# Optimization experiments

Measured on AMD Instinct MI355X. Metric: run time of the kernel, lower is better.

The kernel has to match this reference:

```python
import jax, jax.numpy as jnp
import numpy as np
from jax import lax

NUM_GROUP = 512
GROUP_SIZE = 32


def setup_inputs() -> dict:
    key = jax.random.key(0)
    xyz = jax.random.normal(key, (8, 8192, 6), dtype=jnp.float32)
    return {"xyz": xyz}


def _fps_indices(pts, K):
    """Farthest point sampling. pts: [B,N,3] -> idx [B,K] int32. Start at point 0."""
    B, N, _ = pts.shape
    first = jnp.zeros((B,), dtype=jnp.int32)
    # squared distance of every point to the first selected point
    d = jnp.sum((pts - pts[:, :1, :]) ** 2, axis=-1)  # [B,N]

    def step(d, _):
        nxt = jnp.argmax(d, axis=1).astype(jnp.int32)              # [B]
        newp = jnp.take_along_axis(pts, nxt[:, None, None], axis=1)  # [B,1,3]
        d = jnp.minimum(d, jnp.sum((pts - newp) ** 2, axis=-1))
        return d, nxt

    _, rest = lax.scan(step, d, None, length=K - 1)  # rest: [K-1,B]
    idx = jnp.concatenate([first[None, :], rest], axis=0)  # [K,B]
    return idx.T  # [B,K]


def _group(xyz, num_group, group_size):
    coords = xyz[:, :, :3]    # [B,N,3]
    normals = xyz[:, :, 3:6]  # [B,N,3]

    fps_idx = _fps_indices(coords, num_group)                          # [B,G]
    center = jnp.take_along_axis(coords, fps_idx[:, :, None], axis=1)  # [B,G,3]

    # pairwise squared distances center->points: [B,G,N]
    c2 = jnp.sum(center ** 2, axis=-1)[:, :, None]
    x2 = jnp.sum(coords ** 2, axis=-1)[:, None, :]
    cx = jnp.einsum('bgd,bnd->bgn', center, coords)
    d2 = c2 - 2.0 * cx + x2

    _, knn_idx = lax.top_k(-d2, group_size)  # [B,G,M] nearest neighbors

    flat_idx = knn_idx.reshape(knn_idx.shape[0], -1)  # [B,G*M]
    neigh = jnp.take_along_axis(coords, flat_idx[:, :, None], axis=1)
    neigh = neigh.reshape(-1, num_group, group_size, 3) - center[:, :, None, :]
    neigh_n = jnp.take_along_axis(normals, flat_idx[:, :, None], axis=1)
    neigh_n = neigh_n.reshape(-1, num_group, group_size, 3)
    return neigh, neigh_n, center


def reference(xyz):
    return _group(xyz, NUM_GROUP, GROUP_SIZE)
```

## Files before the change

### kernel.cpp

```cpp
#include <hip/hip_runtime.h>
#include <stdint.h>

#define BATCH 8
#define NPTS 8192
#define NGRP 512
#define GSZ 32
#define NWORK 248
#define CHUNK 16
typedef unsigned long long u64;
typedef float vf2 __attribute__((ext_vector_type(2)));

__device__ __forceinline__ float sq3(float dx, float dy, float dz) {
    return __fadd_rn(__fadd_rn(__fmul_rn(dx, dx), __fmul_rn(dy, dy)), __fmul_rn(dz, dz));
}

template <int C>
__device__ __forceinline__ float dpp_max_f32_step(float v) {
    const int t = __builtin_amdgcn_update_dpp(__float_as_int(v), __float_as_int(v),
                                              C, 0xF, 0xF, false);
    return fmaxf(v, __int_as_float(t));
}
template <int C>
__device__ __forceinline__ unsigned dpp_min_u32_step(unsigned v) {
    const unsigned t = (unsigned)__builtin_amdgcn_update_dpp((int)v, (int)v,
                                                             C, 0xF, 0xF, false);
    return v < t ? v : t;
}
__device__ __forceinline__ float wave_max_f32(float v) {
    v = dpp_max_f32_step<0x111>(v);
    v = dpp_max_f32_step<0x112>(v);
    v = dpp_max_f32_step<0x114>(v);
    v = dpp_max_f32_step<0x118>(v);
    v = dpp_max_f32_step<0x142>(v);
    v = dpp_max_f32_step<0x143>(v);
    return __int_as_float(__builtin_amdgcn_readlane(__float_as_int(v), 63));
}
__device__ __forceinline__ unsigned wave_min_u32(unsigned v) {
    v = dpp_min_u32_step<0x111>(v);
    v = dpp_min_u32_step<0x112>(v);
    v = dpp_min_u32_step<0x114>(v);
    v = dpp_min_u32_step<0x118>(v);
    v = dpp_min_u32_step<0x142>(v);
    v = dpp_min_u32_step<0x143>(v);
    return (unsigned)__builtin_amdgcn_readlane((int)v, 63);
}

__global__ void zero_rc(unsigned* __restrict__ rc) {
    if (threadIdx.x < BATCH) rc[threadIdx.x] = 0;
}

__global__ __launch_bounds__(512) void fused_kernel(const float* __restrict__ xyz,
                                                    float* __restrict__ centers,
                                                    float* __restrict__ neigh,
                                                    float* __restrict__ neigh_n,
                                                    unsigned* __restrict__ rc,
                                                    unsigned* __restrict__ cpx,
                                                    unsigned* __restrict__ cpy,
                                                    unsigned* __restrict__ cpz) {
    __shared__ float4 P4[NPTS];
    __shared__ double pkey[2][8];
    __shared__ float cl[NGRP * 3];
    __shared__ u64 rk[2][8];
    __shared__ int sel[GSZ];

    const int wid = blockIdx.x;
    const int tid = threadIdx.x;
    const int lane = tid & 63;
    const int wv = tid >> 6;

    if (wid < BATCH) {
        const int b = wid;
        vf2 px[8], py[8], pz[8], d2[8];
        const float* base = xyz + (size_t)b * NPTS * 6;

#pragma unroll
        for (int i = 0; i < 16; ++i) {
            const int p = i * 512 + tid;
            const float4 v4 = *reinterpret_cast<const float4*>(base + (size_t)p * 6);
            px[i >> 1][i & 1] = v4.x; py[i >> 1][i & 1] = v4.y; pz[i >> 1][i & 1] = v4.z;
            d2[i >> 1][i & 1] = __int_as_float(0x7f800000);
            P4[p] = make_float4(v4.x, v4.y, v4.z, 0.0f);
        }
        float Bx = base[0], By = base[1], Bz = base[2];
        if (tid == 0) { cl[0] = Bx; cl[1] = By; cl[2] = Bz; }
        __syncthreads();

        for (int k = 1; k < NGRP; ++k) {
            {
#pragma clang fp contract(off)
                const vf2 bx2 = {Bx, Bx}, by2 = {By, By}, bz2 = {Bz, Bz};
#pragma unroll
                for (int j = 0; j < 8; ++j) {
                    const vf2 dx = px[j] - bx2;
                    const vf2 dy = py[j] - by2;
                    const vf2 dz = pz[j] - bz2;
                    const vf2 mx2 = dx * dx;
                    const vf2 my2 = dy * dy;
                    const vf2 mz2 = dz * dz;
                    const vf2 s = (mx2 + my2) + mz2;
                    d2[j] = __builtin_elementwise_min(d2[j], s);
                }
            }
            vf2 mv = d2[0];
#pragma unroll
            for (int j = 1; j < 8; ++j) mv = __builtin_elementwise_max(mv, d2[j]);
            const float mx = fmaxf(mv[0], mv[1]);
            const float wmx = wave_max_f32(mx);
            int wi = 0;
#pragma unroll
            for (int i = 15; i >= 1; --i) {
                wi = (d2[i >> 1][i & 1] == mx) ? i : wi;
            }
            unsigned widx_w;
            const u64 bal = __ballot(mx == wmx);
            if (__popcll(bal) == 1) {
                const int L = __ffsll(bal) - 1;
                widx_w = (unsigned)(__builtin_amdgcn_readlane(wi, L) * 512 + (wv * 64 + L));
            } else {
                const unsigned cand = (mx == wmx) ? (unsigned)(wi * 512 + tid) : 0xFFFFFFFFu;
                widx_w = wave_min_u32(cand);
            }

            const int buf = k & 1;
            if ((tid & 63) == 0) {
                pkey[buf][wv] = __hiloint2double(__float_as_int(wmx), 8191 - (int)widx_w);
            }
            __syncthreads();

            const double2* pp = reinterpret_cast<const double2*>(&pkey[buf][0]);
            const double2 a = pp[0], c = pp[1], e = pp[2], f = pp[3];
            const double g = fmax(fmax(fmax(a.x, a.y), fmax(c.x, c.y)),
                                  fmax(fmax(e.x, e.y), fmax(f.x, f.y)));
            const int widx = 8191 - __double2loint(g);
            const float4 c4 = P4[widx];
            Bx = c4.x; By = c4.y; Bz = c4.z;

            if (tid == 0) {
                cl[k * 3 + 0] = Bx; cl[k * 3 + 1] = By; cl[k * 3 + 2] = Bz;
                if ((k & (CHUNK - 1)) == (CHUNK - 1)) {
                    const int k0 = k - (CHUNK - 1);
#pragma unroll
                    for (int j = 0; j < CHUNK; ++j) {
                        const int kk = k0 + j;
                        const int gi = b * NGRP + kk;
                        __hip_atomic_store(&cpx[gi], __float_as_uint(cl[kk * 3 + 0]),
                                           __ATOMIC_RELAXED, __HIP_MEMORY_SCOPE_AGENT);
                        __hip_atomic_store(&cpy[gi], __float_as_uint(cl[kk * 3 + 1]),
                                           __ATOMIC_RELAXED, __HIP_MEMORY_SCOPE_AGENT);
                        __hip_atomic_store(&cpz[gi], __float_as_uint(cl[kk * 3 + 2]),
                                           __ATOMIC_RELAXED, __HIP_MEMORY_SCOPE_AGENT);
                    }
                    __hip_atomic_store(&rc[b], (unsigned)(k + 1),
                                       __ATOMIC_RELEASE, __HIP_MEMORY_SCOPE_AGENT);
                }
            }
        }

        __syncthreads();
        float* cg = centers + (size_t)b * NGRP * 3;
        for (int t = tid; t < NGRP * 3; t += 512) cg[t] = cl[t];

    } else {
        for (int t = wid - BATCH; t < BATCH * NGRP; t += NWORK) {
            const int b = t & 7, g = t >> 3;
            if (tid == 0) {
                while (__hip_atomic_load(&rc[b], __ATOMIC_ACQUIRE,
                                         __HIP_MEMORY_SCOPE_AGENT) <= (unsigned)g) {
                    __builtin_amdgcn_s_sleep(2);
                }
            }
            __syncthreads();

            const int gi = b * NGRP + g;
            const float cx = __uint_as_float(__hip_atomic_load(
                &cpx[gi], __ATOMIC_RELAXED, __HIP_MEMORY_SCOPE_AGENT));
            const float cy = __uint_as_float(__hip_atomic_load(
                &cpy[gi], __ATOMIC_RELAXED, __HIP_MEMORY_SCOPE_AGENT));
            const float cz = __uint_as_float(__hip_atomic_load(
                &cpz[gi], __ATOMIC_RELAXED, __HIP_MEMORY_SCOPE_AGENT));
            const float c2 = sq3(cx, cy, cz);

            const float* base = xyz + (size_t)b * NPTS * 6;
            u64 key[16];
#pragma unroll
            for (int i = 0; i < 16; ++i) {
                const int p = i * 512 + tid;
                const float4 v4 = *reinterpret_cast<const float4*>(base + (size_t)p * 6);
                const float x = v4.x, y = v4.y, z = v4.z;
                const float x2 = sq3(x, y, z);
                const float dot = __fmaf_rn(cz, z, __fmaf_rn(cy, y, __fmul_rn(cx, x)));
                const float dd = __fadd_rn(__fsub_rn(c2, __fmul_rn(2.0f, dot)), x2);
                unsigned u = __float_as_uint(dd);
                u ^= (unsigned)(((int)u >> 31)) | 0x80000000u;
                key[i] = ((u64)u << 32) | (unsigned)p;
            }

            u64 lm = ~0ULL, lm2v = ~0ULL;
#pragma unroll
            for (int i = 0; i < 16; ++i) {
                const u64 kk = key[i];
                const bool a = kk < lm;
                const bool b2 = kk < lm2v;
                lm2v = a ? lm : (b2 ? kk : lm2v);
                lm = a ? kk : lm;
            }

            for (int r = 0; r < GSZ; ++r) {
                const unsigned hi = (unsigned)(lm >> 32);
                const unsigned minhi = wave_min_u32(hi);
                unsigned minlo;
                const u64 bal = __ballot(hi == minhi);
                if (__popcll(bal) == 1) {
                    const int L = __ffsll(bal) - 1;
                    minlo = (unsigned)__builtin_amdgcn_readlane((int)(unsigned)lm, L);
                } else {
                    const unsigned cand = (hi == minhi) ? (unsigned)lm : 0xFFFFFFFFu;
                    minlo = wave_min_u32(cand);
                }
                const u64 mk = ((u64)minhi << 32) | minlo;

                const int rb = r & 1;
                if (lane == 0) rk[rb][wv] = mk;
                __syncthreads();
                const ulonglong2* rp = reinterpret_cast<const ulonglong2*>(&rk[rb][0]);
                const ulonglong2 r0 = rp[0], r1 = rp[1], r2 = rp[2], r3 = rp[3];
                const u64 m0 = r0.x < r0.y ? r0.x : r0.y;
                const u64 m1 = r1.x < r1.y ? r1.x : r1.y;
                const u64 m2 = r2.x < r2.y ? r2.x : r2.y;
                const u64 m3 = r3.x < r3.y ? r3.x : r3.y;
                const u64 m01 = m0 < m1 ? m0 : m1;
                const u64 m23 = m2 < m3 ? m2 : m3;
                const u64 gm = m01 < m23 ? m01 : m23;
                if (tid == 0) sel[r] = (int)(unsigned)(gm & 0xffffffffu);
                if (lm == gm) {
                    if (lm2v != 0ULL) {
                        lm = lm2v;
                    } else {
                        u64 nm = ~0ULL;
#pragma unroll
                        for (int i = 0; i < 16; ++i) {
                            const u64 v = key[i] > gm ? key[i] : ~0ULL;
                            nm = v < nm ? v : nm;
                        }
                        lm = nm;
                    }
                    lm2v = 0ULL;
                }
            }
            __syncthreads();

            if (tid < GSZ) {
                const int idx = sel[tid];
                const float* q = base + (size_t)idx * 6;
                const float4 a4 = *reinterpret_cast<const float4*>(q);
                const float2 b2v = *reinterpret_cast<const float2*>(q + 4);
                const int row = b * NGRP + g;
                const size_t o = ((size_t)row * GSZ + tid) * 3;
                neigh[o + 0] = __fsub_rn(a4.x, cx);
                neigh[o + 1] = __fsub_rn(a4.y, cy);
                neigh[o + 2] = __fsub_rn(a4.z, cz);
                neigh_n[o + 0] = a4.w;
                neigh_n[o + 1] = b2v.x;
                neigh_n[o + 2] = b2v.y;
            }
        }
    }
}

extern "C" void kernel_launch(void* const* d_in, const int* in_sizes, int n_in,
                              void* d_out, int out_size, void* d_ws, size_t ws_size,
                              hipStream_t stream) {
    const float* xyz = (const float*)d_in[0];
    float* out = (float*)d_out;
    float* neigh   = out;
    float* neigh_n = out + (size_t)BATCH * NGRP * GSZ * 3;
    float* centers = out + (size_t)2 * BATCH * NGRP * GSZ * 3;

    unsigned* rc  = (unsigned*)d_ws;
    unsigned* cpx = (unsigned*)((char*)d_ws + 1024);
    unsigned* cpy = (unsigned*)((char*)d_ws + 1024 + 16384);
    unsigned* cpz = (unsigned*)((char*)d_ws + 1024 + 32768);

    zero_rc<<<1, 64, 0, stream>>>(rc);
    fused_kernel<<<BATCH + NWORK, 512, 0, stream>>>(xyz, centers, neigh, neigh_n,
                                                    rc, cpx, cpy, cpz);
}
```

Before: 547.9 us.

## Publish FPS centers in parallel with lagged release and fewer consumer blocks

The FPS producer now publishes each finished chunk of centers from 48 threads in parallel, using an interleaved xyz buffer instead of three separate arrays. It releases the ready counter one chunk late, taking the serial per-center stores off thread 0's critical path inside the FPS loop. Consumer blocks drop from 248 to 120 and back off longer while polling, which cuts memory traffic from spinning that could slow the latency-bound FPS loop. The trade-off is fewer workers for the kNN phase and later availability of each center chunk, which could lengthen the tail after FPS finishes.

```diff
diff --git a/kernel.cpp b/kernel.cpp
--- a/kernel.cpp
+++ b/kernel.cpp
@@ -5,7 +5,7 @@
 #define NPTS 8192
 #define NGRP 512
 #define GSZ 32
-#define NWORK 248
+#define NWORK 120
 #define CHUNK 16
 typedef unsigned long long u64;
 typedef float vf2 __attribute__((ext_vector_type(2)));
@@ -54,9 +54,7 @@
                                                     float* __restrict__ neigh,
                                                     float* __restrict__ neigh_n,
                                                     unsigned* __restrict__ rc,
-                                                    unsigned* __restrict__ cpx,
-                                                    unsigned* __restrict__ cpy,
-                                                    unsigned* __restrict__ cpz) {
+                                                    unsigned* __restrict__ cp) {
     __shared__ float4 P4[NPTS];
     __shared__ double pkey[2][8];
     __shared__ float cl[NGRP * 3];
@@ -127,6 +125,18 @@
             }
             __syncthreads();
 
+            if ((k & (CHUNK - 1)) == 0) {
+                if (tid == 0 && k >= 2 * CHUNK) {
+                    __hip_atomic_store(&rc[b], (unsigned)(k - CHUNK),
+                                       __ATOMIC_RELEASE, __HIP_MEMORY_SCOPE_AGENT);
+                }
+                if (tid < 3 * CHUNK) {
+                    const int j = (k - CHUNK) * 3 + tid;
+                    __hip_atomic_store(&cp[b * NGRP * 3 + j], __float_as_uint(cl[j]),
+                                       __ATOMIC_RELAXED, __HIP_MEMORY_SCOPE_AGENT);
+                }
+            }
+
             const double2* pp = reinterpret_cast<const double2*>(&pkey[buf][0]);
             const double2 a = pp[0], c = pp[1], e = pp[2], f = pp[3];
             const double g = fmax(fmax(fmax(a.x, a.y), fmax(c.x, c.y)),
@@ -135,30 +145,22 @@
             const float4 c4 = P4[widx];
             Bx = c4.x; By = c4.y; Bz = c4.z;
 
-            if (tid == 0) {
-                cl[k * 3 + 0] = Bx; cl[k * 3 + 1] = By; cl[k * 3 + 2] = Bz;
-                if ((k & (CHUNK - 1)) == (CHUNK - 1)) {
-                    const int k0 = k - (CHUNK - 1);
-#pragma unroll
-                    for (int j = 0; j < CHUNK; ++j) {
-                        const int kk = k0 + j;
-                        const int gi = b * NGRP + kk;
-                        __hip_atomic_store(&cpx[gi], __float_as_uint(cl[kk * 3 + 0]),
-                                           __ATOMIC_RELAXED, __HIP_MEMORY_SCOPE_AGENT);
-                        __hip_atomic_store(&cpy[gi], __float_as_uint(cl[kk * 3 + 1]),
-                                           __ATOMIC_RELAXED, __HIP_MEMORY_SCOPE_AGENT);
-                        __hip_atomic_store(&cpz[gi], __float_as_uint(cl[kk * 3 + 2]),
-                                           __ATOMIC_RELAXED, __HIP_MEMORY_SCOPE_AGENT);
-                    }
-                    __hip_atomic_store(&rc[b], (unsigned)(k + 1),
-                                       __ATOMIC_RELEASE, __HIP_MEMORY_SCOPE_AGENT);
-                }
-            }
+            if (tid == 0) { cl[k * 3 + 0] = Bx; cl[k * 3 + 1] = By; cl[k * 3 + 2] = Bz; }
         }
 
         __syncthreads();
         float* cg = centers + (size_t)b * NGRP * 3;
-        for (int t = tid; t < NGRP * 3; t += 512) cg[t] = cl[t];
+        for (int t2 = tid; t2 < NGRP * 3; t2 += 512) cg[t2] = cl[t2];
+        if (tid < 3 * CHUNK) {
+            const int j = (NGRP - CHUNK) * 3 + tid;
+            __hip_atomic_store(&cp[b * NGRP * 3 + j], __float_as_uint(cl[j]),
+                               __ATOMIC_RELAXED, __HIP_MEMORY_SCOPE_AGENT);
+        }
+        __syncthreads();
+        if (tid == 0) {
+            __hip_atomic_store(&rc[b], (unsigned)NGRP,
+                               __ATOMIC_RELEASE, __HIP_MEMORY_SCOPE_AGENT);
+        }
 
     } else {
         for (int t = wid - BATCH; t < BATCH * NGRP; t += NWORK) {
@@ -166,18 +168,18 @@
             if (tid == 0) {
                 while (__hip_atomic_load(&rc[b], __ATOMIC_ACQUIRE,
                                          __HIP_MEMORY_SCOPE_AGENT) <= (unsigned)g) {
-                    __builtin_amdgcn_s_sleep(2);
+                    __builtin_amdgcn_s_sleep(64);
                 }
             }
             __syncthreads();
 
-            const int gi = b * NGRP + g;
+            const int gi = (b * NGRP + g) * 3;
             const float cx = __uint_as_float(__hip_atomic_load(
-                &cpx[gi], __ATOMIC_RELAXED, __HIP_MEMORY_SCOPE_AGENT));
+                &cp[gi + 0], __ATOMIC_RELAXED, __HIP_MEMORY_SCOPE_AGENT));
             const float cy = __uint_as_float(__hip_atomic_load(
-                &cpy[gi], __ATOMIC_RELAXED, __HIP_MEMORY_SCOPE_AGENT));
+                &cp[gi + 1], __ATOMIC_RELAXED, __HIP_MEMORY_SCOPE_AGENT));
             const float cz = __uint_as_float(__hip_atomic_load(
-                &cpz[gi], __ATOMIC_RELAXED, __HIP_MEMORY_SCOPE_AGENT));
+                &cp[gi + 2], __ATOMIC_RELAXED, __HIP_MEMORY_SCOPE_AGENT));
             const float c2 = sq3(cx, cy, cz);
 
             const float* base = xyz + (size_t)b * NPTS * 6;
@@ -276,12 +278,10 @@
     float* neigh_n = out + (size_t)BATCH * NGRP * GSZ * 3;
     float* centers = out + (size_t)2 * BATCH * NGRP * GSZ * 3;
 
-    unsigned* rc  = (unsigned*)d_ws;
-    unsigned* cpx = (unsigned*)((char*)d_ws + 1024);
-    unsigned* cpy = (unsigned*)((char*)d_ws + 1024 + 16384);
-    unsigned* cpz = (unsigned*)((char*)d_ws + 1024 + 32768);
+    unsigned* rc = (unsigned*)d_ws;
+    unsigned* cp = (unsigned*)((char*)d_ws + 1024);
 
     zero_rc<<<1, 64, 0, stream>>>(rc);
     fused_kernel<<<BATCH + NWORK, 512, 0, stream>>>(xyz, centers, neigh, neigh_n,
-                                                    rc, cpx, cpy, cpz);
-}
+                                                    rc, cp);
+}
```

After: 732.0 us. 33.6% more time.
